# Performance work log

Hardware: AMD Instinct MI355X
Metric: run time of the kernel (lower is better)

Reference implementation:

```python
import jax, jax.numpy as jnp
import numpy as np

TAU = 1.0
NUM_NEURONS = 32768
INPUT_SIZE = 8192
BATCH = 512


def setup_inputs() -> dict:
    key = jax.random.key(0)
    k1, k2, k3 = jax.random.split(key, 3)
    x = jax.random.uniform(k1, (BATCH, INPUT_SIZE), dtype=jnp.float32)
    gate_weights = jax.random.normal(k2, (NUM_NEURONS, 16), dtype=jnp.float32)
    input_idx = jax.random.randint(k3, (NUM_NEURONS, 2), 0, INPUT_SIZE, dtype=jnp.int32)
    return {"x": x, "gate_weights": gate_weights, "input_idx": input_idx}


def _all_logic_ops(a, b):
    # 16 soft (real-valued) binary logic gates, stacked on last axis.
    ab = a * b
    one = jnp.ones_like(a)
    zero = jnp.zeros_like(a)
    return jnp.stack([
        zero,                  # FALSE
        ab,                    # a AND b
        a - ab,                # a AND NOT b
        a,                     # a
        b - ab,                # NOT a AND b
        b,                     # b
        a + b - 2.0 * ab,      # a XOR b
        a + b - ab,            # a OR b
        1.0 - (a + b - ab),    # NOR
        1.0 - (a + b - 2.0 * ab),  # XNOR
        1.0 - b,               # NOT b
        1.0 - b + ab,          # a OR NOT b
        1.0 - a,               # NOT a
        1.0 - a + ab,          # NOT a OR b
        1.0 - ab,              # NAND
        one,                   # TRUE
    ], axis=-1)  # (B, N, 16)


def reference(x, gate_weights, input_idx):
    # gather the two input columns per neuron: (B, N)
    a = x[:, input_idx[:, 0]]
    b = x[:, input_idx[:, 1]]
    ops = _all_logic_ops(a, b)                          # (B, N, 16)
    w = jax.nn.softmax(gate_weights / TAU, axis=1)      # (N, 16)
    out = jnp.einsum('bnk,nk->bn', ops, w)              # (B, N)
    return out
```

## Files before the change

### kernel.cpp

```cpp
#include <hip/hip_runtime.h>
#include <hip/hip_bf16.h>

#define NUM_NEURONS 32768
#define INPUT_SIZE  8192
#define BATCH       512

typedef float f32x4 __attribute__((ext_vector_type(4)));

__global__ __launch_bounds__(256) void logic_coeff_kernel(
    const float* __restrict__ gw, float4* __restrict__ coeffs)
{
    const int n = blockIdx.x * 256 + threadIdx.x;
    if (n >= NUM_NEURONS) return;
    const float* g = gw + (size_t)n * 16;

    float w[16];
#pragma unroll
    for (int i = 0; i < 16; i += 4) {
        float4 v = *reinterpret_cast<const float4*>(g + i);
        w[i+0] = v.x; w[i+1] = v.y; w[i+2] = v.z; w[i+3] = v.w;
    }
    float m = w[0];
#pragma unroll
    for (int i = 1; i < 16; ++i) m = fmaxf(m, w[i]);
    float s = 0.f;
#pragma unroll
    for (int i = 0; i < 16; ++i) { w[i] = __expf(w[i] - m); s += w[i]; }
    const float inv = 1.0f / s;

    const float C0  = (w[8] + w[9] + w[10] + w[11] + w[12] + w[13] + w[14] + w[15]) * inv;
    const float Ca  = (w[2] + w[3] + w[6] + w[7] - w[8] - w[9] - w[12] - w[13]) * inv;
    const float Cb  = (w[4] + w[5] + w[6] + w[7] - w[8] - w[9] - w[10] - w[11]) * inv;
    const float Cab = (w[1] - w[2] - w[4] - 2.f*w[6] - w[7]
                       + w[8] + 2.f*w[9] + w[11] + w[13] - w[14]) * inv;

    coeffs[n] = make_float4(C0, Ca, Cb, Cab);
}

constexpr int RPB = 2;
constexpr int BLK = 1024;
constexpr int QPT = NUM_NEURONS / 4 / BLK;
constexpr int SF4 = RPB * INPUT_SIZE / 4 / BLK;

__global__ __launch_bounds__(BLK, 4) void logic_main_kernel(
    const float*  __restrict__ x,
    const float4* __restrict__ coeffs,
    const int4*   __restrict__ idx4,
    float*        __restrict__ out)
{
    __shared__ float sx[RPB][INPUT_SIZE];

    const int tid  = threadIdx.x;
    const int row0 = blockIdx.x * RPB;

    {
        const float4* xr = reinterpret_cast<const float4*>(x + (size_t)row0 * INPUT_SIZE);
        float4* s4 = reinterpret_cast<float4*>(&sx[0][0]);
#pragma unroll
        for (int i = 0; i < SF4; ++i) {
            __builtin_amdgcn_global_load_lds(
                (const __attribute__((address_space(1))) void*)(xr + i * BLK + tid),
                (__attribute__((address_space(3))) void*)(s4 + i * BLK + tid),
                16, 0, 0);
        }
    }
    asm volatile("s_waitcnt vmcnt(0)" ::: "memory");
    __builtin_amdgcn_s_barrier();

#pragma unroll 2
    for (int g = 0; g < QPT; ++g) {
        const int nb = g * (BLK * 4) + tid * 4;

        const float4 c0 = coeffs[nb + 0];
        const float4 c1 = coeffs[nb + 1];
        const float4 c2 = coeffs[nb + 2];
        const float4 c3 = coeffs[nb + 3];
        const int4   p0 = idx4[(nb >> 1) + 0];
        const int4   p1 = idx4[(nb >> 1) + 1];

#pragma unroll
        for (int rr = 0; rr < RPB; ++rr) {
            const float* s = sx[rr];
            f32x4 res;
            {
                const float a = s[p0.x], b = s[p0.y];
                res[0] = fmaf(a, fmaf(c0.w, b, c0.y), fmaf(c0.z, b, c0.x));
            }
            {
                const float a = s[p0.z], b = s[p0.w];
                res[1] = fmaf(a, fmaf(c1.w, b, c1.y), fmaf(c1.z, b, c1.x));
            }
            {
                const float a = s[p1.x], b = s[p1.y];
                res[2] = fmaf(a, fmaf(c2.w, b, c2.y), fmaf(c2.z, b, c2.x));
            }
            {
                const float a = s[p1.z], b = s[p1.w];
                res[3] = fmaf(a, fmaf(c3.w, b, c3.y), fmaf(c3.z, b, c3.x));
            }
            __builtin_nontemporal_store(
                res, reinterpret_cast<f32x4*>(out + (size_t)(row0 + rr) * NUM_NEURONS + nb));
        }
    }
}

extern "C" void kernel_launch(void* const* d_in, const int* in_sizes, int n_in,
                              void* d_out, int out_size, void* d_ws, size_t ws_size,
                              hipStream_t stream)
{
    const float* x   = (const float*)d_in[0];
    const float* gw  = (const float*)d_in[1];
    const int4*  idx = (const int4*)d_in[2];
    float* out = (float*)d_out;

    float4* coeffs = (float4*)d_ws;

    logic_coeff_kernel<<<NUM_NEURONS / 256, 256, 0, stream>>>(gw, coeffs);

    logic_main_kernel<<<BATCH / RPB, BLK, 0, stream>>>(x, coeffs, idx, out);
}
```

Measured before the change: 94.78 us.

## Split neuron range across two blocks per row pair and stagger wave chunk order

```diff
diff --git a/kernel.cpp b/kernel.cpp
--- a/kernel.cpp
+++ b/kernel.cpp
@@ -37,10 +37,11 @@
     coeffs[n] = make_float4(C0, Ca, Cb, Cab);
 }
 
-constexpr int RPB = 2;
-constexpr int BLK = 1024;
-constexpr int QPT = NUM_NEURONS / 4 / BLK;
-constexpr int SF4 = RPB * INPUT_SIZE / 4 / BLK;
+constexpr int BLK  = 512;
+constexpr int RPB  = 2;
+constexpr int HALF = NUM_NEURONS / 2;
+constexpr int QPT  = HALF / 4 / BLK;
+constexpr int SF4  = RPB * INPUT_SIZE / 4 / BLK;
 
 __global__ __launch_bounds__(BLK, 4) void logic_main_kernel(
     const float*  __restrict__ x,
@@ -51,7 +52,11 @@
     __shared__ float sx[RPB][INPUT_SIZE];
 
     const int tid  = threadIdx.x;
-    const int row0 = blockIdx.x * RPB;
+    const int bid  = blockIdx.x;
+    const int rp   = bid & 255;
+    const int half = bid >> 8;
+    const int row0 = rp * RPB;
+    const int nh0  = half * HALF;
 
     {
         const float4* xr = reinterpret_cast<const float4*>(x + (size_t)row0 * INPUT_SIZE);
@@ -67,9 +72,16 @@
     asm volatile("s_waitcnt vmcnt(0)" ::: "memory");
     __builtin_amdgcn_s_barrier();
 
+    const int wid  = tid >> 6;
+    const int lane = tid & 63;
+
+    float* o0 = out + (size_t)row0 * NUM_NEURONS;
+    float* o1 = o0 + NUM_NEURONS;
+
 #pragma unroll 2
-    for (int g = 0; g < QPT; ++g) {
-        const int nb = g * (BLK * 4) + tid * 4;
+    for (int it = 0; it < QPT; ++it) {
+        const int g  = (it + wid) & (QPT - 1);
+        const int nb = nh0 + g * 2048 + wid * 256 + lane * 4;
 
         const float4 c0 = coeffs[nb + 0];
         const float4 c1 = coeffs[nb + 1];
@@ -78,28 +90,31 @@
         const int4   p0 = idx4[(nb >> 1) + 0];
         const int4   p1 = idx4[(nb >> 1) + 1];
 
-#pragma unroll
-        for (int rr = 0; rr < RPB; ++rr) {
-            const float* s = sx[rr];
+        {
+            const float* s = sx[0];
             f32x4 res;
-            {
-                const float a = s[p0.x], b = s[p0.y];
-                res[0] = fmaf(a, fmaf(c0.w, b, c0.y), fmaf(c0.z, b, c0.x));
-            }
-            {
-                const float a = s[p0.z], b = s[p0.w];
-                res[1] = fmaf(a, fmaf(c1.w, b, c1.y), fmaf(c1.z, b, c1.x));
-            }
-            {
-                const float a = s[p1.x], b = s[p1.y];
-                res[2] = fmaf(a, fmaf(c2.w, b, c2.y), fmaf(c2.z, b, c2.x));
-            }
-            {
-                const float a = s[p1.z], b = s[p1.w];
-                res[3] = fmaf(a, fmaf(c3.w, b, c3.y), fmaf(c3.z, b, c3.x));
-            }
-            __builtin_nontemporal_store(
-                res, reinterpret_cast<f32x4*>(out + (size_t)(row0 + rr) * NUM_NEURONS + nb));
+            { const float a = s[p0.x], b = s[p0.y];
+              res[0] = fmaf(a, fmaf(c0.w, b, c0.y), fmaf(c0.z, b, c0.x)); }
+            { const float a = s[p0.z], b = s[p0.w];
+              res[1] = fmaf(a, fmaf(c1.w, b, c1.y), fmaf(c1.z, b, c1.x)); }
+            { const float a = s[p1.x], b = s[p1.y];
+              res[2] = fmaf(a, fmaf(c2.w, b, c2.y), fmaf(c2.z, b, c2.x)); }
+            { const float a = s[p1.z], b = s[p1.w];
+              res[3] = fmaf(a, fmaf(c3.w, b, c3.y), fmaf(c3.z, b, c3.x)); }
+            __builtin_nontemporal_store(res, reinterpret_cast<f32x4*>(o0 + nb));
+        }
+        {
+            const float* s = sx[1];
+            f32x4 res;
+            { const float a = s[p0.x], b = s[p0.y];
+              res[0] = fmaf(a, fmaf(c0.w, b, c0.y), fmaf(c0.z, b, c0.x)); }
+            { const float a = s[p0.z], b = s[p0.w];
+              res[1] = fmaf(a, fmaf(c1.w, b, c1.y), fmaf(c1.z, b, c1.x)); }
+            { const float a = s[p1.x], b = s[p1.y];
+              res[2] = fmaf(a, fmaf(c2.w, b, c2.y), fmaf(c2.z, b, c2.x)); }
+            { const float a = s[p1.z], b = s[p1.w];
+              res[3] = fmaf(a, fmaf(c3.w, b, c3.y), fmaf(c3.z, b, c3.x)); }
+            __builtin_nontemporal_store(res, reinterpret_cast<f32x4*>(o1 + nb));
         }
     }
 }
@@ -117,5 +132,5 @@
 
     logic_coeff_kernel<<<NUM_NEURONS / 256, 256, 0, stream>>>(gw, coeffs);
 
-    logic_main_kernel<<<BATCH / RPB, BLK, 0, stream>>>(x, coeffs, idx, out);
+    logic_main_kernel<<<(BATCH / RPB) * 2, BLK, 0, stream>>>(x, coeffs, idx, out);
 }
```

Result: faster. 92.45 us (-2.5%).
